# Optimization experiments

Hardware: AMD Instinct MI355X
Metric: run time of the kernel (lower is better)

## Reference

```python
import jax, jax.numpy as jnp
import numpy as np

B, N, C = 8, 729, 1152
H, D = 16, 72          # num_heads, head_dim (C = H*D)
F = 4304               # intermediate_size
R = 23                 # ToMe merge count r
EPS = 1e-6
SCALE = D ** -0.5


def _ln(x, g, b):
    m = jnp.mean(x, axis=-1, keepdims=True)
    v = jnp.var(x, axis=-1, keepdims=True)
    return (x - m) * jax.lax.rsqrt(v + EPS) * g + b


def _tome_merge_wavg(metric, x, r):
    """ToMe bipartite soft matching + weighted-average merge (size=None -> ones).
    metric: [B,N,D] per-token key mean; x: [B,N,C]. Returns [B, N-r, C]."""
    m = metric / jnp.linalg.norm(metric, axis=-1, keepdims=True)
    a, bm = m[:, ::2], m[:, 1::2]                       # [B,Na,D],[B,Nb,D]
    scores = jnp.einsum('bnd,bmd->bnm', a, bm)          # cosine sims [B,Na,Nb]
    node_max = jnp.max(scores, axis=-1)                 # [B,Na]
    node_idx = jnp.argmax(scores, axis=-1)              # best dst per src
    edge_idx = jnp.argsort(-node_max, axis=-1)          # descending similarity
    unm_idx = edge_idx[:, r:]                           # unmerged src tokens
    src_idx = edge_idx[:, :r]                           # merged src tokens
    dst_idx = jnp.take_along_axis(node_idx, src_idx, axis=1)  # [B,r]

    size = jnp.ones(x.shape[:2] + (1,), x.dtype)

    def merge_sum(t):
        src, dst = t[:, ::2], t[:, 1::2]
        unm = jnp.take_along_axis(src, unm_idx[..., None], axis=1)
        sel = jnp.take_along_axis(src, src_idx[..., None], axis=1)
        dst = jax.vmap(lambda d, i, s: d.at[i].add(s))(dst, dst_idx, sel)
        return jnp.concatenate([unm, dst], axis=1)

    xs = merge_sum(x * size)
    ss = merge_sum(size)
    return xs / ss


def setup_inputs() -> dict:
    key = jax.random.key(0)
    ks = jax.random.split(key, 16)
    s = 0.02
    inp = {
        'hidden_states': jax.random.normal(ks[0], (B, N, C), jnp.float32),
        'attention_mask': 0.1 * jax.random.normal(ks[1], (B, 1, N, N), jnp.float32),
        'wq': s * jax.random.normal(ks[2], (C, C), jnp.float32),
        'bq': jnp.zeros((C,), jnp.float32),
        'wk': s * jax.random.normal(ks[3], (C, C), jnp.float32),
        'bk': jnp.zeros((C,), jnp.float32),
        'wv': s * jax.random.normal(ks[4], (C, C), jnp.float32),
        'bv': jnp.zeros((C,), jnp.float32),
        'wo': s * jax.random.normal(ks[5], (C, C), jnp.float32),
        'bo': jnp.zeros((C,), jnp.float32),
        'ln1_w': jnp.ones((C,), jnp.float32),
        'ln1_b': jnp.zeros((C,), jnp.float32),
        'ln2_w': jnp.ones((C,), jnp.float32),
        'ln2_b': jnp.zeros((C,), jnp.float32),
        'fc1_w': s * jax.random.normal(ks[6], (C, F), jnp.float32),
        'fc1_b': jnp.zeros((F,), jnp.float32),
        'fc2_w': s * jax.random.normal(ks[7], (F, C), jnp.float32),
        'fc2_b': jnp.zeros((C,), jnp.float32),
    }
    return inp


def reference(hidden_states, attention_mask, wq, bq, wk, bk, wv, bv, wo, bo,
              ln1_w, ln1_b, ln2_w, ln2_b, fc1_w, fc1_b, fc2_w, fc2_b):
    residual = hidden_states
    x = _ln(hidden_states, ln1_w, ln1_b)

    q = (x @ wq + bq).reshape(B, N, H, D)
    k = (x @ wk + bk).reshape(B, N, H, D)
    v = (x @ wv + bv).reshape(B, N, H, D)

    metric = jnp.mean(k, axis=2)                        # [B,N,D] (mean over heads)

    scores = jnp.einsum('bqhd,bkhd->bhqk', q, k) * SCALE
    scores = scores + attention_mask                    # [B,1,N,N] broadcast bias
    attn = jax.nn.softmax(scores.astype(jnp.float32), axis=-1).astype(q.dtype)
    out = jnp.einsum('bhqk,bkhd->bqhd', attn, v).reshape(B, N, C)
    attn_out = out @ wo + bo

    h = residual + attn_out
    h = _tome_merge_wavg(metric, h, R)                  # [B, N-R, C]

    residual = h
    h = _ln(h, ln2_w, ln2_b)
    h = jax.nn.gelu(h @ fc1_w + fc1_b, approximate=True)  # gelu_pytorch_tanh
    h = h @ fc2_w + fc2_b
    return residual + h
```

## Files before the change

### kernel.cpp

```cpp
#include <hip/hip_runtime.h>
#include <hip/hip_bf16.h>
#include <math.h>

namespace {

constexpr int Bn = 8;
constexpr int Nn = 729;
constexpr int Cn = 1152;
constexpr int Hn = 16;
constexpr int Dn = 72;
constexpr int Fn = 4304;
constexpr int Rn = 23;
constexpr int NAn = 365;
constexpr int NBn = 364;
constexpr int NMn = 706;
constexpr int UNMn = NAn - Rn;
constexpr float EPSf = 1e-6f;
constexpr float SCALEf = 0.11785113019775793f;

using bf16 = __hip_bfloat16;
typedef short v8s __attribute__((ext_vector_type(8)));
typedef float v4f __attribute__((ext_vector_type(4)));

__device__ __forceinline__ float toF(bf16 v) { return __bfloat162float(v); }
__device__ __forceinline__ void stF(float* p, float v) { *p = v; }
__device__ __forceinline__ void stF(bf16* p, float v) { *p = __float2bfloat16(v); }

__device__ __forceinline__ float geluf(float x) {
  float x3 = x * x * x;
  return 0.5f * x * (1.f + tanhf(0.7978845608028654f * (x + 0.044715f * x3)));
}

__device__ __forceinline__ int clampi(int v, int lo, int hi) {
  return v < lo ? lo : (v > hi ? hi : v);
}

__device__ __forceinline__ void gl_lds16(const bf16* __restrict__ g, short* l) {
  __builtin_amdgcn_global_load_lds(
      (const __attribute__((address_space(1))) void*)g,
      (__attribute__((address_space(3))) void*)l, 16, 0, 0);
}

__global__ __launch_bounds__(256) void ln_stats_kernel(const float* __restrict__ x,
                                                       float* __restrict__ sf,
                                                       double* __restrict__ sd,
                                                       int rows) {
  int row = blockIdx.x;
  if (row >= rows) return;
  const float* xr = x + (size_t)row * Cn;
  double s = 0.0, s2 = 0.0;
  for (int c = threadIdx.x; c < Cn; c += 256) {
    double v = (double)xr[c];
    s += v; s2 += v * v;
  }
  __shared__ double sh[8];
#pragma unroll
  for (int o = 32; o > 0; o >>= 1) { s += __shfl_down(s, o); s2 += __shfl_down(s2, o); }
  int w = threadIdx.x >> 6;
  if ((threadIdx.x & 63) == 0) { sh[w] = s; sh[4 + w] = s2; }
  __syncthreads();
  if (threadIdx.x == 0) {
    double ts = sh[0] + sh[1] + sh[2] + sh[3];
    double ts2 = sh[4] + sh[5] + sh[6] + sh[7];
    double mean = ts / Cn;
    double var = ts2 / Cn - mean * mean;
    double rstd = 1.0 / sqrt(var + (double)EPSf);
    sf[2 * row] = (float)mean;
    sf[2 * row + 1] = (float)rstd;
    if (sd) { sd[2 * row] = mean; sd[2 * row + 1] = rstd; }
  }
}

__global__ __launch_bounds__(256) void ln_apply_kernel(const float* __restrict__ x,
                                                       const float* __restrict__ stats,
                                                       const float* __restrict__ g,
                                                       const float* __restrict__ b,
                                                       bf16* __restrict__ y) {
  int row = blockIdx.x;
  float mean = stats[2 * row], rstd = stats[2 * row + 1];
  const float* xr = x + (size_t)row * Cn;
  bf16* yr = y + (size_t)row * Cn;
  for (int c = threadIdx.x; c < Cn; c += 256)
    yr[c] = __float2bfloat16((xr[c] - mean) * rstd * g[c] + b[c]);
}

__global__ __launch_bounds__(256) void wconv_kernel(const float* __restrict__ W,
                                                    bf16* __restrict__ Wt,
                                                    int K, int N, float scale) {
  __shared__ float tile[32][33];
  int kt = blockIdx.y * 32, nt = blockIdx.x * 32;
  int tx = threadIdx.x & 31, ty = threadIdx.x >> 5;
#pragma unroll
  for (int yy = 0; yy < 4; ++yy) {
    int k = kt + ty * 4 + yy, n = nt + tx;
    tile[ty * 4 + yy][tx] = (k < K && n < N) ? W[(size_t)k * N + n] : 0.f;
  }
  __syncthreads();
#pragma unroll
  for (int yy = 0; yy < 4; ++yy) {
    int n = nt + ty * 4 + yy, k = kt + tx;
    if (n < N && k < K) Wt[(size_t)n * K + k] = __float2bfloat16(tile[tx][ty * 4 + yy] * scale);
  }
}

__global__ __launch_bounds__(256) void vscale_kernel(const float* __restrict__ in,
                                                     float* __restrict__ out, int n, float s) {
  int i = blockIdx.x * 256 + threadIdx.x;
  if (i < n) out[i] = in[i] * s;
}

template <typename OT, int BT>
__global__ __launch_bounds__(256) void mfma_gemm(const bf16* __restrict__ A,
                                                 const bf16* __restrict__ Wt,
                                                 const float* __restrict__ bias,
                                                 const float* __restrict__ resid,
                                                 OT* __restrict__ Cout,
                                                 int M, int N, int K, int act) {
  constexpr int FR = BT / 32;
  constexpr int WL = BT / 64;
  __align__(16) __shared__ short As[BT * 32];
  __align__(16) __shared__ short Bs[BT * 32];
  int bm = blockIdx.y * BT, bn = blockIdx.x * BT;
  int tid = threadIdx.x;
  int lane = tid & 63, w = tid >> 6;
  int wm = w >> 1, wn = w & 1;
  int l16 = lane & 15, quad = lane >> 4;
  int srow = tid >> 2, skc = (tid & 3) * 8;
  int lr = lane >> 2, lc8 = (lane & 3) * 8;
  bool interior = (bm + BT <= M) && (bn + BT <= N);
  v4f acc[FR][FR];
#pragma unroll
  for (int i = 0; i < FR; ++i)
#pragma unroll
    for (int j = 0; j < FR; ++j) acc[i][j] = (v4f){0.f, 0.f, 0.f, 0.f};
  int ksteps = (K + 31) / 32;
  for (int ks = 0; ks < ksteps; ++ks) {
    int k0 = ks * 32;
    __syncthreads();
    if (interior && (k0 + 32 <= K)) {
#pragma unroll
      for (int h2 = 0; h2 < WL; ++h2) {
        int rb = (w + h2 * 4) * 16;
        int r = rb + lr;
        gl_lds16(A + (size_t)(bm + r) * K + k0 + lc8, &As[rb * 32]);
        gl_lds16(Wt + (size_t)(bn + r) * K + k0 + lc8, &Bs[rb * 32]);
      }
    } else {
#pragma unroll
      for (int h2 = 0; h2 < WL; ++h2) {
        int r = srow + h2 * 64;
        int4 za = {0, 0, 0, 0}, zb = {0, 0, 0, 0};
        if (k0 + skc < K) {
          if (bm + r < M) za = *reinterpret_cast<const int4*>(A + (size_t)(bm + r) * K + k0 + skc);
          if (bn + r < N) zb = *reinterpret_cast<const int4*>(Wt + (size_t)(bn + r) * K + k0 + skc);
        }
        *reinterpret_cast<int4*>(&As[r * 32 + skc]) = za;
        *reinterpret_cast<int4*>(&Bs[r * 32 + skc]) = zb;
      }
    }
    __syncthreads();
    v8s af[FR], bfr[FR];
#pragma unroll
    for (int i = 0; i < FR; ++i)
      af[i] = *reinterpret_cast<const v8s*>(&As[(wm * (BT / 2) + i * 16 + l16) * 32 + quad * 8]);
#pragma unroll
    for (int j = 0; j < FR; ++j)
      bfr[j] = *reinterpret_cast<const v8s*>(&Bs[(wn * (BT / 2) + j * 16 + l16) * 32 + quad * 8]);
#pragma unroll
    for (int i = 0; i < FR; ++i)
#pragma unroll
      for (int j = 0; j < FR; ++j)
        acc[i][j] = __builtin_amdgcn_mfma_f32_16x16x32_bf16(af[i], bfr[j], acc[i][j], 0, 0, 0);
  }
#pragma unroll
  for (int i = 0; i < FR; ++i) {
#pragma unroll
    for (int j = 0; j < FR; ++j) {
#pragma unroll
      for (int r = 0; r < 4; ++r) {
        int row = bm + wm * (BT / 2) + i * 16 + quad * 4 + r;
        int col = bn + wn * (BT / 2) + j * 16 + l16;
        if (row < M && col < N) {
          float v = acc[i][j][r] + bias[col];
          if (act) v = geluf(v);
          if (resid) v += resid[(size_t)row * N + col];
          stF(&Cout[(size_t)row * N + col], v);
        }
      }
    }
  }
}

constexpr int NKP = 768;
__global__ __launch_bounds__(256) void vtrans_kernel(const bf16* __restrict__ v,
                                                     bf16* __restrict__ vt) {
  int kb = blockIdx.x % 12;
  int bh = blockIdx.x / 12;
  int h = bh % Hn, b = bh / Hn;
  __shared__ short Ts[64][73];
  int tid = threadIdx.x;
#pragma unroll
  for (int i = 0; i < 18; ++i) {
    int idx = tid + i * 256;
    int key = idx / 72, d = idx % 72;
    int kg = kb * 64 + key;
    bf16 val = (kg < Nn) ? v[((size_t)(b * Nn + kg)) * Cn + h * Dn + d] : bf16(0.f);
    Ts[key][d] = *reinterpret_cast<short*>(&val);
  }
  __syncthreads();
#pragma unroll
  for (int i = 0; i < 18; ++i) {
    int idx = tid + i * 256;
    int d = idx / 64, key = idx % 64;
    vt[((size_t)bh * 80 + d) * NKP + kb * 64 + key] = *reinterpret_cast<bf16*>(&Ts[key][d]);
  }
  for (int i = tid; i < 8 * 64; i += 256) {
    int d = 72 + i / 64, key = i % 64;
    vt[((size_t)bh * 80 + d) * NKP + kb * 64 + key] = bf16(0.f);
  }
}

constexpr int ATQ = 64, ATK = 64;
constexpr int NQT2 = (Nn + ATQ - 1) / ATQ;
constexpr int NKT = 12;
constexpr int KSS = 104, VTS = 72, PSS = 72;

__device__ __forceinline__ void attn_load_tile(const bf16* __restrict__ k,
                                               const bf16* __restrict__ vt,
                                               int b, int bh, int h, int kt_, int tid,
                                               int4* kr, int4* vr) {
#pragma unroll
  for (int i = 0; i < 3; ++i) {
    int idx = tid + i * 256;
    int r = idx / 12, ch = idx % 12;
    int kg = kt_ + r;
    int4 z = {0, 0, 0, 0};
    if (ch < 9 && kg < Nn)
      z = *reinterpret_cast<const int4*>(k + ((size_t)(b * Nn + kg)) * Cn + h * Dn + ch * 8);
    kr[i] = z;
    if (idx < 640) {
      int d = idx >> 3, kc = idx & 7;
      vr[i] = *reinterpret_cast<const int4*>(vt + ((size_t)bh * 80 + d) * NKP + kt_ + kc * 8);
    }
  }
}

__global__ __launch_bounds__(256) void attn_mfma_kernel(bf16* q ,
                                                        const bf16* __restrict__ k,
                                                        const bf16* __restrict__ vt,
                                                        const float* __restrict__ mask) {
  int blk = blockIdx.x;
  int b = blk & 7;
  int r0 = blk >> 3;
  int h = r0 / NQT2;
  int qt = r0 % NQT2;
  int bh = b * Hn + h;
  __align__(16) __shared__ short Ks[ATK * KSS];
  __align__(16) __shared__ short Vt[80 * VTS];
  __align__(16) __shared__ short Ps[4][16 * PSS];
  int tid = threadIdx.x;
  int lane = tid & 63, w = tid >> 6;
  int l16 = lane & 15, quad = lane >> 4;

  v8s aq[3];
  int qg_l = qt * ATQ + w * 16 + l16;
  {
    const bf16* qrow = q + ((size_t)(b * Nn + (qg_l < Nn ? qg_l : 0))) * Cn + h * Dn;
#pragma unroll
    for (int ks = 0; ks < 3; ++ks) {
      bool valid = (qg_l < Nn) && (ks < 2 || quad == 0);
      if (valid)
        aq[ks] = *reinterpret_cast<const v8s*>(qrow + ks * 32 + quad * 8);
      else
        aq[ks] = (v8s){0, 0, 0, 0, 0, 0, 0, 0};
    }
  }

  v4f o[5];
#pragma unroll
  for (int dj = 0; dj < 5; ++dj) o[dj] = (v4f){0.f, 0.f, 0.f, 0.f};
  float m_r[4] = {-INFINITY, -INFINITY, -INFINITY, -INFINITY};
  float l_r[4] = {0.f, 0.f, 0.f, 0.f};

  int4 kr[3], vr[3];
  attn_load_tile(k, vt, b, bh, h, 0, tid, kr, vr);

  for (int t = 0; t < NKT; ++t) {
    int kt2 = t * ATK;
    __syncthreads();
#pragma unroll
    for (int i = 0; i < 3; ++i) {
      int idx = tid + i * 256;
      int r = idx / 12, ch = idx % 12;
      *reinterpret_cast<int4*>(&Ks[r * KSS + ch * 8]) = kr[i];
      if (idx < 640) {
        int d = idx >> 3, kc = idx & 7;
        *reinterpret_cast<int4*>(&Vt[d * VTS + kc * 8]) = vr[i];
      }
    }
    __syncthreads();
    if (t + 1 < NKT) attn_load_tile(k, vt, b, bh, h, kt2 + ATK, tid, kr, vr);

    v4f sfr[4];
#pragma unroll
    for (int j = 0; j < 4; ++j) sfr[j] = (v4f){0.f, 0.f, 0.f, 0.f};
#pragma unroll
    for (int ks = 0; ks < 3; ++ks) {
#pragma unroll
      for (int j = 0; j < 4; ++j) {
        v8s bk_ = *reinterpret_cast<const v8s*>(&Ks[(j * 16 + l16) * KSS + ks * 32 + quad * 8]);
        sfr[j] = __builtin_amdgcn_mfma_f32_16x16x32_bf16(aq[ks], bk_, sfr[j], 0, 0, 0);
      }
    }
    float sv[4][4];
    int qbase = qt * ATQ + w * 16 + quad * 4;
    bool tfull = (kt2 + ATK <= Nn);
#pragma unroll
    for (int r = 0; r < 4; ++r) {
      int qg = qbase + r;
      const float* mrow = mask + ((size_t)(b * Nn + (qg < Nn ? qg : 0))) * Nn;
      if (tfull && qg < Nn) {
#pragma unroll
        for (int j = 0; j < 4; ++j) sv[j][r] = sfr[j][r] + mrow[kt2 + j * 16 + l16];
      } else {
#pragma unroll
        for (int j = 0; j < 4; ++j) {
          int kg = kt2 + j * 16 + l16;
          sv[j][r] = (kg < Nn && qg < Nn) ? sfr[j][r] + mrow[kg] : -INFINITY;
        }
      }
    }
    float alpha[4];
#pragma unroll
    for (int r = 0; r < 4; ++r) {
      float mx = fmaxf(fmaxf(sv[0][r], sv[1][r]), fmaxf(sv[2][r], sv[3][r]));
#pragma unroll
      for (int o2 = 1; o2 < 16; o2 <<= 1) mx = fmaxf(mx, __shfl_xor(mx, o2));
      float mnew = fmaxf(m_r[r], mx);
      float ps = 0.f;
#pragma unroll
      for (int j = 0; j < 4; ++j) {
        float p = __expf(sv[j][r] - mnew);
        bf16 pb = __float2bfloat16(p);
        Ps[w][(quad * 4 + r) * PSS + j * 16 + l16] = *reinterpret_cast<short*>(&pb);
        ps += p;
      }
      alpha[r] = __expf(m_r[r] - mnew);
      l_r[r] = l_r[r] * alpha[r] + ps;
      m_r[r] = mnew;
    }
#pragma unroll
    for (int dj = 0; dj < 5; ++dj)
#pragma unroll
      for (int r = 0; r < 4; ++r) o[dj][r] *= alpha[r];
#pragma unroll
    for (int st = 0; st < 2; ++st) {
      v8s ap = *reinterpret_cast<const v8s*>(&Ps[w][l16 * PSS + st * 32 + quad * 8]);
#pragma unroll
      for (int dj = 0; dj < 5; ++dj) {
        v8s bv_ = *reinterpret_cast<const v8s*>(&Vt[(dj * 16 + l16) * VTS + st * 32 + quad * 8]);
        o[dj] = __builtin_amdgcn_mfma_f32_16x16x32_bf16(ap, bv_, o[dj], 0, 0, 0);
      }
    }
  }
  float linv[4];
#pragma unroll
  for (int r = 0; r < 4; ++r) {
    float lt = l_r[r];
#pragma unroll
    for (int o2 = 1; o2 < 16; o2 <<= 1) lt += __shfl_xor(lt, o2);
    linv[r] = (lt > 0.f) ? 1.f / lt : 0.f;
  }
#pragma unroll
  for (int dj = 0; dj < 5; ++dj) {
    int d = dj * 16 + l16;
    if (d >= Dn) continue;
#pragma unroll
    for (int r = 0; r < 4; ++r) {
      int qg = qt * ATQ + w * 16 + quad * 4 + r;
      if (qg < Nn)
        q[((size_t)(b * Nn + qg)) * Cn + h * Dn + d] = __float2bfloat16(o[dj][r] * linv[r]);
    }
  }
}

__global__ __launch_bounds__(128) void wkavg_kernel(const float* __restrict__ wk,
                                                    const float* __restrict__ bk,
                                                    double* __restrict__ wka,
                                                    double* __restrict__ bka) {
  int c = blockIdx.x;
  int d = threadIdx.x;
  if (d < Dn) {
    double s = 0.0;
    for (int h = 0; h < Hn; ++h) s += (double)wk[(size_t)c * Cn + h * Dn + d];
    wka[(size_t)c * Dn + d] = s / Hn;
    if (c == 0) {
      double t = 0.0;
      for (int h = 0; h < Hn; ++h) t += (double)bk[h * Dn + d];
      bka[d] = t / Hn;
    }
  }
}

constexpr int MT_ROWS = 64;
constexpr int MT_KT = 32;
constexpr int MT_SK = 3;
constexpr int MT_KC = Cn / MT_SK;
__global__ __launch_bounds__(256) void metric_gemm_kernel(const float* __restrict__ x,
                                                          const double* __restrict__ sd,
                                                          const float* __restrict__ g,
                                                          const float* __restrict__ b,
                                                          const double* __restrict__ wka,
                                                          double* __restrict__ kpart,
                                                          int rows) {
  int row0 = blockIdx.x * MT_ROWS;
  int k0base = blockIdx.y * MT_KC;
  __shared__ double As[MT_ROWS][MT_KT + 1];
  __shared__ double Ws[MT_KT][Dn];
  __shared__ double smean[MT_ROWS], srstd[MT_ROWS];
  int tid = threadIdx.x;
  int rg = tid >> 3;
  int dg = tid & 7;
  int d0 = dg * 9;
  if (tid < MT_ROWS) {
    int r = row0 + tid;
    smean[tid] = (r < rows) ? sd[2 * r] : 0.0;
    srstd[tid] = (r < rows) ? sd[2 * r + 1] : 0.0;
  }
  double acc0[9], acc1[9];
#pragma unroll
  for (int j = 0; j < 9; ++j) { acc0[j] = 0.0; acc1[j] = 0.0; }
  __syncthreads();
  for (int kt = 0; kt < MT_KC; kt += MT_KT) {
    int k0 = k0base + kt;
    __syncthreads();
#pragma unroll
    for (int i = 0; i < 8; ++i) {
      int idx = tid + i * 256;
      int c = idx & 31, r = idx >> 5;
      int gr = row0 + r;
      double a = 0.0;
      if (gr < rows) {
        double xv = (double)x[(size_t)gr * Cn + k0 + c];
        a = (xv - smean[r]) * srstd[r] * (double)g[k0 + c] + (double)b[k0 + c];
      }
      As[r][c] = a;
    }
#pragma unroll
    for (int i = 0; i < 9; ++i) {
      int idx = tid + i * 256;
      int c = idx / Dn, d = idx % Dn;
      Ws[c][d] = wka[(size_t)(k0 + c) * Dn + d];
    }
    __syncthreads();
#pragma unroll 2
    for (int c = 0; c < MT_KT; ++c) {
      double a0 = As[rg * 2][c], a1 = As[rg * 2 + 1][c];
#pragma unroll
      for (int j = 0; j < 9; ++j) {
        double wv = Ws[c][d0 + j];
        acc0[j] += a0 * wv;
        acc1[j] += a1 * wv;
      }
    }
  }
  size_t base = (size_t)blockIdx.y * rows;
  int r0g = row0 + rg * 2;
#pragma unroll
  for (int j = 0; j < 9; ++j) {
    if (r0g < rows) kpart[(base + r0g) * Dn + d0 + j] = acc0[j];
    if (r0g + 1 < rows) kpart[(base + r0g + 1) * Dn + d0 + j] = acc1[j];
  }
}

__global__ __launch_bounds__(128) void metric_norm_kernel(const double* __restrict__ kpart,
                                                          const double* __restrict__ bka,
                                                          double* __restrict__ mn,
                                                          int rows) {
  int row = blockIdx.x;
  __shared__ double red[Dn];
  __shared__ double nrm;
  int d = threadIdx.x;
  double v = 0.0;
  if (d < Dn) {
    v = kpart[(size_t)row * Dn + d]
      + kpart[((size_t)rows + row) * Dn + d]
      + kpart[((size_t)2 * rows + row) * Dn + d]
      + bka[d];
    red[d] = v * v;
  }
  __syncthreads();
  if (threadIdx.x == 0) {
    double t = 0.0;
    for (int i = 0; i < Dn; ++i) t += red[i];
    nrm = 1.0 / sqrt(t > 0.0 ? t : 1e-300);
  }
  __syncthreads();
  if (d < Dn) mn[(size_t)row * Dn + d] = v * nrm;
}

__global__ __launch_bounds__(128) void tome_score_kernel(const double* __restrict__ mn,
                                                         double* __restrict__ nmax,
                                                         int* __restrict__ nidx) {
  int blk = blockIdx.x;
  int i = blk % NAn;
  int b = blk / NAn;
  __shared__ double av[Dn];
  __shared__ double sv[128];
  __shared__ int si[128];
  int tid = threadIdx.x;
  if (tid < Dn) av[tid] = mn[((size_t)(b * Nn) + 2 * i) * Dn + tid];
  __syncthreads();
  double best = -1e300;
  int bi = 0;
  for (int c2 = tid; c2 < NBn; c2 += 128) {
    const double* bv = mn + ((size_t)(b * Nn) + 2 * c2 + 1) * Dn;
    double s = 0.0;
#pragma unroll 8
    for (int dd = 0; dd < Dn; ++dd) s += av[dd] * bv[dd];
    if (s > best) { best = s; bi = c2; }
  }
  sv[tid] = best;
  si[tid] = bi;
  __syncthreads();
  if (tid == 0) {
    double bb = sv[0];
    int ii = si[0];
    for (int t2 = 1; t2 < 128; ++t2) {
      if (sv[t2] > bb || (sv[t2] == bb && si[t2] < ii)) { bb = sv[t2]; ii = si[t2]; }
    }
    nmax[b * NAn + i] = bb;
    nidx[b * NAn + i] = clampi(ii, 0, NBn - 1);
  }
}

__global__ __launch_bounds__(512) void tome_sort_kernel(const double* __restrict__ nmax,
                                                        const int* __restrict__ nidx,
                                                        int* __restrict__ unm,
                                                        int* __restrict__ srcI,
                                                        int* __restrict__ dstI,
                                                        float* __restrict__ cnt) {
  int b = blockIdx.x;
  __shared__ double v[NAn];
  __shared__ int eidx[NAn];
  __shared__ int dsts[Rn];
  int tid = threadIdx.x;
  for (int i = tid; i < NAn; i += blockDim.x) {
    v[i] = nmax[b * NAn + i];
    eidx[i] = i;
  }
  __syncthreads();
  for (int i = tid; i < NAn; i += blockDim.x) {
    double vi = v[i];
    int rank = 0;
    for (int j = 0; j < NAn; ++j) {
      double vj = v[j];
      rank += (vj > vi) || (vj == vi && j < i);
    }
    eidx[clampi(rank, 0, NAn - 1)] = i;
  }
  __syncthreads();
  for (int r2 = tid; r2 < NAn; r2 += blockDim.x) {
    if (r2 >= Rn) unm[(size_t)b * UNMn + (r2 - Rn)] = clampi(eidx[r2], 0, NAn - 1);
  }
  if (tid < Rn) {
    int s = clampi(eidx[tid], 0, NAn - 1);
    srcI[b * Rn + tid] = s;
    int dd = clampi(nidx[b * NAn + s], 0, NBn - 1);
    dsts[tid] = dd;
    dstI[b * Rn + tid] = dd;
  }
  for (int j = tid; j < NBn; j += blockDim.x) cnt[(size_t)b * NBn + j] = 1.f;
  __syncthreads();
  if (tid == 0) {
    for (int r2 = 0; r2 < Rn; ++r2) cnt[(size_t)b * NBn + dsts[r2]] += 1.f;
  }
}

__global__ __launch_bounds__(256) void tome_merge_kernel(const float* __restrict__ h,
                                                         const int* __restrict__ unm,
                                                         const int* __restrict__ srcI,
                                                         const int* __restrict__ dstI,
                                                         const float* __restrict__ cnt,
                                                         float* __restrict__ mg) {
  int blk = blockIdx.x;
  int t = blk % NMn;
  int b = blk / NMn;
  __shared__ int s_src[Rn], s_dst[Rn];
  if (threadIdx.x < Rn) {
    s_src[threadIdx.x] = clampi(srcI[b * Rn + threadIdx.x], 0, NAn - 1);
    s_dst[threadIdx.x] = clampi(dstI[b * Rn + threadIdx.x], 0, NBn - 1);
  }
  __syncthreads();
  if (t < UNMn) {
    int tok = clampi(2 * clampi(unm[(size_t)b * UNMn + t], 0, NAn - 1), 0, Nn - 1);
    for (int c = threadIdx.x; c < Cn; c += 256)
      mg[((size_t)(b * NMn + t)) * Cn + c] = h[((size_t)(b * Nn + tok)) * Cn + c];
  } else {
    int j = t - UNMn;
    int tok = 2 * j + 1;
    float inv = 1.f / cnt[b * NBn + j];
    for (int c = threadIdx.x; c < Cn; c += 256) {
      float vsum = h[((size_t)(b * Nn + tok)) * Cn + c];
      for (int r2 = 0; r2 < Rn; ++r2)
        if (s_dst[r2] == j) vsum += h[((size_t)(b * Nn + 2 * s_src[r2])) * Cn + c];
      mg[((size_t)(b * NMn + t)) * Cn + c] = vsum * inv;
    }
  }
}

inline int cdiv(int a, int b) { return (a + b - 1) / b; }

}

extern "C" void kernel_launch(void* const* d_in, const int* in_sizes, int n_in,
                              void* d_out, int out_size, void* d_ws, size_t ws_size,
                              hipStream_t stream) {
  const float* hidden = (const float*)d_in[0];
  const float* mask   = (const float*)d_in[1];
  const float* wq = (const float*)d_in[2];
  const float* bq = (const float*)d_in[3];
  const float* wk = (const float*)d_in[4];
  const float* bk = (const float*)d_in[5];
  const float* wv = (const float*)d_in[6];
  const float* bv = (const float*)d_in[7];
  const float* wo = (const float*)d_in[8];
  const float* bo = (const float*)d_in[9];
  const float* ln1w = (const float*)d_in[10];
  const float* ln1b = (const float*)d_in[11];
  const float* ln2w = (const float*)d_in[12];
  const float* ln2b = (const float*)d_in[13];
  const float* fc1w = (const float*)d_in[14];
  const float* fc1b = (const float*)d_in[15];
  const float* fc2w = (const float*)d_in[16];
  const float* fc2b = (const float*)d_in[17];
  float* out = (float*)d_out;
  (void)in_sizes; (void)n_in; (void)out_size;

  char* ws = (char*)d_ws;
  size_t off = 0;
  auto alloc = [&](size_t nbytes) -> void* {
    void* p = ws + off;
    off += (nbytes + 255) & ~(size_t)255;
    return p;
  };
  int rows = Bn * Nn;
  int mrows = Bn * NMn;
  size_t bnc = (size_t)rows * Cn;
  bf16* wqT = (bf16*)alloc((size_t)Cn * Cn * 2);
  bf16* wkT = (bf16*)alloc((size_t)Cn * Cn * 2);
  bf16* wvT = (bf16*)alloc((size_t)Cn * Cn * 2);
  bf16* woT = (bf16*)alloc((size_t)Cn * Cn * 2);
  bf16* fc1T = (bf16*)alloc((size_t)Fn * Cn * 2);
  bf16* fc2T = (bf16*)alloc((size_t)Cn * Fn * 2);
  bf16* xlnB = (bf16*)alloc(bnc * 2);
  bf16* qb = (bf16*)alloc(bnc * 2);
  bf16* kb = (bf16*)alloc(bnc * 2);
  bf16* vb = (bf16*)alloc(bnc * 2);
  bf16* h2B = (bf16*)alloc((size_t)mrows * Cn * 2);
  double* mnD = (double*)alloc((size_t)rows * Dn * 8);
  double* wkavgD = (double*)alloc((size_t)Cn * Dn * 8);
  double* bkavgD = (double*)alloc((size_t)Dn * 8);
  float* stats1f = (float*)alloc((size_t)rows * 2 * 4);
  double* stats1d = (double*)alloc((size_t)rows * 2 * 8);
  float* stats2f = (float*)alloc((size_t)mrows * 2 * 4);
  double* nmaxD = (double*)alloc((size_t)Bn * NAn * 8);
  int* nidx = (int*)alloc((size_t)Bn * NAn * 4);
  int* unm  = (int*)alloc((size_t)Bn * UNMn * 4);
  int* srcI = (int*)alloc((size_t)Bn * Rn * 4);
  int* dstI = (int*)alloc((size_t)Bn * Rn * 4);
  float* cnt = (float*)alloc((size_t)Bn * NBn * 4);
  float* bqS = (float*)alloc((size_t)Cn * 4);
  bf16* ffnB = (bf16*)(ws + off);
  size_t remain = (ws_size > off) ? (ws_size - off) : 0;
  size_t fullB = (size_t)mrows * Fn * 2;
  int CHUNK = (remain >= fullB) ? mrows : 2824;
  float* hbuf = (float*)kb;
  float* mg   = (float*)xlnB;
  bf16* vtG   = ffnB;
  double* kpartD = (double*)ffnB;

  wconv_kernel<<<dim3(cdiv(Cn, 32), cdiv(Cn, 32)), 256, 0, stream>>>(wq, wqT, Cn, Cn, SCALEf);
  wconv_kernel<<<dim3(cdiv(Cn, 32), cdiv(Cn, 32)), 256, 0, stream>>>(wk, wkT, Cn, Cn, 1.f);
  wconv_kernel<<<dim3(cdiv(Cn, 32), cdiv(Cn, 32)), 256, 0, stream>>>(wv, wvT, Cn, Cn, 1.f);
  wconv_kernel<<<dim3(cdiv(Cn, 32), cdiv(Cn, 32)), 256, 0, stream>>>(wo, woT, Cn, Cn, 1.f);
  wconv_kernel<<<dim3(cdiv(Fn, 32), cdiv(Cn, 32)), 256, 0, stream>>>(fc1w, fc1T, Cn, Fn, 1.f);
  wconv_kernel<<<dim3(cdiv(Cn, 32), cdiv(Fn, 32)), 256, 0, stream>>>(fc2w, fc2T, Fn, Cn, 1.f);
  vscale_kernel<<<cdiv(Cn, 256), 256, 0, stream>>>(bq, bqS, Cn, SCALEf);

  ln_stats_kernel<<<rows, 256, 0, stream>>>(hidden, stats1f, stats1d, rows);

  wkavg_kernel<<<Cn, 128, 0, stream>>>(wk, bk, wkavgD, bkavgD);
  metric_gemm_kernel<<<dim3(cdiv(rows, MT_ROWS), MT_SK), 256, 0, stream>>>(
      hidden, stats1d, ln1w, ln1b, wkavgD, kpartD, rows);
  metric_norm_kernel<<<rows, 128, 0, stream>>>(kpartD, bkavgD, mnD, rows);
  tome_score_kernel<<<Bn * NAn, 128, 0, stream>>>(mnD, nmaxD, nidx);
  tome_sort_kernel<<<Bn, 512, 0, stream>>>(nmaxD, nidx, unm, srcI, dstI, cnt);

  ln_apply_kernel<<<rows, 256, 0, stream>>>(hidden, stats1f, ln1w, ln1b, xlnB);

  dim3 g64(cdiv(Cn, 64), cdiv(rows, 64));
  mfma_gemm<bf16, 64><<<g64, 256, 0, stream>>>(xlnB, wqT, bqS, nullptr, qb, rows, Cn, Cn, 0);
  mfma_gemm<bf16, 64><<<g64, 256, 0, stream>>>(xlnB, wkT, bk, nullptr, kb, rows, Cn, Cn, 0);
  mfma_gemm<bf16, 64><<<g64, 256, 0, stream>>>(xlnB, wvT, bv, nullptr, vb, rows, Cn, Cn, 0);

  vtrans_kernel<<<Bn * Hn * 12, 256, 0, stream>>>(vb, vtG);

  attn_mfma_kernel<<<Bn * Hn * NQT2, 256, 0, stream>>>(qb, kb, vtG, mask);

  mfma_gemm<float, 64><<<g64, 256, 0, stream>>>(qb, woT, bo, hidden, hbuf, rows, Cn, Cn, 0);

  tome_merge_kernel<<<Bn * NMn, 256, 0, stream>>>(hbuf, unm, srcI, dstI, cnt, mg);

  ln_stats_kernel<<<mrows, 256, 0, stream>>>(mg, stats2f, (double*)nullptr, mrows);
  ln_apply_kernel<<<mrows, 256, 0, stream>>>(mg, stats2f, ln2w, ln2b, h2B);

  for (int c0 = 0; c0 < mrows; c0 += CHUNK) {
    int m = (mrows - c0 < CHUNK) ? (mrows - c0) : CHUNK;
    dim3 gf1(cdiv(Fn, 128), cdiv(m, 128));
    mfma_gemm<bf16, 128><<<gf1, 256, 0, stream>>>(h2B + (size_t)c0 * Cn, fc1T, fc1b, nullptr,
                                                  ffnB, m, Fn, Cn, 1);
    dim3 gf2(cdiv(Cn, 64), cdiv(m, 64));
    mfma_gemm<float, 64><<<gf2, 256, 0, stream>>>(ffnB, fc2T, fc2b, mg + (size_t)c0 * Cn,
                                                  out + (size_t)c0 * Cn, m, Cn, Fn, 0);
  }
}
```

Measured before the change: 1.133 ms.

## Fuse QKV projections into one GEMM and add XCD-aware grouped tile swizzle

```diff
diff --git a/kernel.cpp b/kernel.cpp
--- a/kernel.cpp
+++ b/kernel.cpp
@@ -115,12 +115,28 @@
                                                  const float* __restrict__ bias,
                                                  const float* __restrict__ resid,
                                                  OT* __restrict__ Cout,
+                                                 OT* __restrict__ C2,
+                                                 OT* __restrict__ C3,
                                                  int M, int N, int K, int act) {
   constexpr int FR = BT / 32;
   constexpr int WL = BT / 64;
+  constexpr int GM = 6;
   __align__(16) __shared__ short As[BT * 32];
   __align__(16) __shared__ short Bs[BT * 32];
-  int bm = blockIdx.y * BT, bn = blockIdx.x * BT;
+  int nx = (N + BT - 1) / BT, ny = (M + BT - 1) / BT;
+  int nwg = nx * ny;
+  int blk = blockIdx.x;
+  int q8 = nwg >> 3, r8 = nwg & 7;
+  int xcd = blk & 7, slot = blk >> 3;
+  int wgid = (xcd < r8 ? xcd * (q8 + 1) : r8 * (q8 + 1) + (xcd - r8) * q8) + slot;
+  int npg = GM * nx;
+  int gid = wgid / npg;
+  int rem = wgid - gid * npg;
+  int m0 = gid * GM;
+  int gsz = ny - m0; if (gsz > GM) gsz = GM;
+  int by = m0 + rem % gsz;
+  int bx = rem / gsz;
+  int bm = by * BT, bn = bx * BT;
   int tid = threadIdx.x;
   int lane = tid & 63, w = tid >> 6;
   int wm = w >> 1, wn = w & 1;
@@ -172,6 +188,7 @@
       for (int j = 0; j < FR; ++j)
         acc[i][j] = __builtin_amdgcn_mfma_f32_16x16x32_bf16(af[i], bfr[j], acc[i][j], 0, 0, 0);
   }
+  int w3 = C2 ? (N / 3) : 0;
 #pragma unroll
   for (int i = 0; i < FR; ++i) {
 #pragma unroll
@@ -184,7 +201,13 @@
           float v = acc[i][j][r] + bias[col];
           if (act) v = geluf(v);
           if (resid) v += resid[(size_t)row * N + col];
-          stF(&Cout[(size_t)row * N + col], v);
+          if (C2) {
+            int seg = col / w3, c2 = col - seg * w3;
+            OT* d = (seg == 0) ? Cout : (seg == 1 ? C2 : C3);
+            stF(&d[(size_t)row * w3 + c2], v);
+          } else {
+            stF(&Cout[(size_t)row * N + col], v);
+          }
         }
       }
     }
@@ -647,9 +670,10 @@
   int rows = Bn * Nn;
   int mrows = Bn * NMn;
   size_t bnc = (size_t)rows * Cn;
-  bf16* wqT = (bf16*)alloc((size_t)Cn * Cn * 2);
-  bf16* wkT = (bf16*)alloc((size_t)Cn * Cn * 2);
-  bf16* wvT = (bf16*)alloc((size_t)Cn * Cn * 2);
+  bf16* wqkvT = (bf16*)alloc((size_t)3 * Cn * Cn * 2);
+  bf16* wqT = wqkvT;
+  bf16* wkT = wqkvT + (size_t)Cn * Cn;
+  bf16* wvT = wqkvT + (size_t)2 * Cn * Cn;
   bf16* woT = (bf16*)alloc((size_t)Cn * Cn * 2);
   bf16* fc1T = (bf16*)alloc((size_t)Fn * Cn * 2);
   bf16* fc2T = (bf16*)alloc((size_t)Cn * Fn * 2);
@@ -670,7 +694,7 @@
   int* srcI = (int*)alloc((size_t)Bn * Rn * 4);
   int* dstI = (int*)alloc((size_t)Bn * Rn * 4);
   float* cnt = (float*)alloc((size_t)Bn * NBn * 4);
-  float* bqS = (float*)alloc((size_t)Cn * 4);
+  float* bqkv = (float*)alloc((size_t)3 * Cn * 4);
   bf16* ffnB = (bf16*)(ws + off);
   size_t remain = (ws_size > off) ? (ws_size - off) : 0;
   size_t fullB = (size_t)mrows * Fn * 2;
@@ -686,7 +710,9 @@
   wconv_kernel<<<dim3(cdiv(Cn, 32), cdiv(Cn, 32)), 256, 0, stream>>>(wo, woT, Cn, Cn, 1.f);
   wconv_kernel<<<dim3(cdiv(Fn, 32), cdiv(Cn, 32)), 256, 0, stream>>>(fc1w, fc1T, Cn, Fn, 1.f);
   wconv_kernel<<<dim3(cdiv(Cn, 32), cdiv(Fn, 32)), 256, 0, stream>>>(fc2w, fc2T, Fn, Cn, 1.f);
-  vscale_kernel<<<cdiv(Cn, 256), 256, 0, stream>>>(bq, bqS, Cn, SCALEf);
+  vscale_kernel<<<cdiv(Cn, 256), 256, 0, stream>>>(bq, bqkv, Cn, SCALEf);
+  vscale_kernel<<<cdiv(Cn, 256), 256, 0, stream>>>(bk, bqkv + Cn, Cn, 1.f);
+  vscale_kernel<<<cdiv(Cn, 256), 256, 0, stream>>>(bv, bqkv + 2 * Cn, Cn, 1.f);
 
   ln_stats_kernel<<<rows, 256, 0, stream>>>(hidden, stats1f, stats1d, rows);
 
@@ -699,16 +725,21 @@
 
   ln_apply_kernel<<<rows, 256, 0, stream>>>(hidden, stats1f, ln1w, ln1b, xlnB);
 
-  dim3 g64(cdiv(Cn, 64), cdiv(rows, 64));
-  mfma_gemm<bf16, 64><<<g64, 256, 0, stream>>>(xlnB, wqT, bqS, nullptr, qb, rows, Cn, Cn, 0);
-  mfma_gemm<bf16, 64><<<g64, 256, 0, stream>>>(xlnB, wkT, bk, nullptr, kb, rows, Cn, Cn, 0);
-  mfma_gemm<bf16, 64><<<g64, 256, 0, stream>>>(xlnB, wvT, bv, nullptr, vb, rows, Cn, Cn, 0);
+  {
+    int nx = cdiv(3 * Cn, 64), ny = cdiv(rows, 64);
+    mfma_gemm<bf16, 64><<<nx * ny, 256, 0, stream>>>(xlnB, wqkvT, bqkv, nullptr,
+                                                     qb, kb, vb, rows, 3 * Cn, Cn, 0);
+  }
 
   vtrans_kernel<<<Bn * Hn * 12, 256, 0, stream>>>(vb, vtG);
 
   attn_mfma_kernel<<<Bn * Hn * NQT2, 256, 0, stream>>>(qb, kb, vtG, mask);
 
-  mfma_gemm<float, 64><<<g64, 256, 0, stream>>>(qb, woT, bo, hidden, hbuf, rows, Cn, Cn, 0);
+  {
+    int nx = cdiv(Cn, 64), ny = cdiv(rows, 64);
+    mfma_gemm<float, 64><<<nx * ny, 256, 0, stream>>>(qb, woT, bo, hidden,
+                                                      hbuf, nullptr, nullptr, rows, Cn, Cn, 0);
+  }
 
   tome_merge_kernel<<<Bn * NMn, 256, 0, stream>>>(hbuf, unm, srcI, dstI, cnt, mg);
 
@@ -717,11 +748,17 @@
 
   for (int c0 = 0; c0 < mrows; c0 += CHUNK) {
     int m = (mrows - c0 < CHUNK) ? (mrows - c0) : CHUNK;
-    dim3 gf1(cdiv(Fn, 128), cdiv(m, 128));
-    mfma_gemm<bf16, 128><<<gf1, 256, 0, stream>>>(h2B + (size_t)c0 * Cn, fc1T, fc1b, nullptr,
-                                                  ffnB, m, Fn, Cn, 1);
-    dim3 gf2(cdiv(Cn, 64), cdiv(m, 64));
-    mfma_gemm<float, 64><<<gf2, 256, 0, stream>>>(ffnB, fc2T, fc2b, mg + (size_t)c0 * Cn,
-                                                  out + (size_t)c0 * Cn, m, Cn, Fn, 0);
-  }
-}
+    {
+      int nx = cdiv(Fn, 128), ny = cdiv(m, 128);
+      mfma_gemm<bf16, 128><<<nx * ny, 256, 0, stream>>>(h2B + (size_t)c0 * Cn, fc1T, fc1b,
+                                                        nullptr, ffnB, nullptr, nullptr,
+                                                        m, Fn, Cn, 1);
+    }
+    {
+      int nx = cdiv(Cn, 64), ny = cdiv(m, 64);
+      mfma_gemm<float, 64><<<nx * ny, 256, 0, stream>>>(ffnB, fc2T, fc2b, mg + (size_t)c0 * Cn,
+                                                        out + (size_t)c0 * Cn, nullptr, nullptr,
+                                                        m, Cn, Fn, 0);
+    }
+  }
+}
```

Result: faster. 1.088 ms (-4.0%).
